# Performance work log

Measured on AMD Instinct MI355X. Metric: run time of the kernel, lower is better.

The kernel has to match this reference:

```python
import jax, jax.numpy as jnp
import numpy as np

B, C, N, IC = 4, 64, 4096, 32  # batch, in_channels(=g_channels), nodes, inter_channels


def setup_inputs() -> dict:
    key = jax.random.key(0)
    ks = jax.random.split(key, 8)
    s_c = (2.0 / C) ** 0.5   # kaiming-ish scales
    s_i = (2.0 / C) ** 0.5
    x = jax.random.normal(ks[0], (B, C, N), dtype=jnp.float32)
    g_w = jax.random.normal(ks[1], (C, C), dtype=jnp.float32) * s_c      # g: 1x1 conv (out=C, in=C)
    g_b = jnp.zeros((C,), dtype=jnp.float32)
    theta_w = jax.random.normal(ks[2], (IC, C), dtype=jnp.float32) * s_i  # theta: (out=IC, in=C)
    theta_b = jnp.zeros((IC,), dtype=jnp.float32)
    phi_w = jax.random.normal(ks[3], (IC, C), dtype=jnp.float32) * s_i
    phi_b = jnp.zeros((IC,), dtype=jnp.float32)
    cp_w = jax.random.normal(ks[4], (2 * IC,), dtype=jnp.float32) * (2.0 / (2 * IC)) ** 0.5  # concat_project 1x1 conv, no bias
    C_k = jnp.zeros((N, N), dtype=jnp.float32)  # learned adjacency bias, init zeros
    return {"x": x, "g_w": g_w, "g_b": g_b, "theta_w": theta_w, "theta_b": theta_b,
            "phi_w": phi_w, "phi_b": phi_b, "cp_w": cp_w, "C_k": C_k}


def reference(x, g_w, g_b, theta_w, theta_b, phi_w, phi_b, cp_w, C_k):
    # 1x1 convs are plain GEMMs over the node dim
    g_x = jnp.einsum('oc,bcn->bno', g_w, x) + g_b            # (B, N, C)
    th = jnp.einsum('oc,bcn->bon', theta_w, x) + theta_b[:, None]  # (B, IC, N)
    ph = jnp.einsum('oc,bcn->bon', phi_w, x) + phi_b[:, None]      # (B, IC, N)
    # concat_project on [theta_i ; phi_j] with a 1x1 conv is algebraically an outer sum:
    # f[b,i,j] = w_th . theta[b,:,i] + w_ph . phi[b,:,j]
    a = jnp.einsum('c,bcn->bn', cp_w[:IC], th)  # (B, N)
    p = jnp.einsum('c,bcn->bn', cp_w[IC:], ph)  # (B, N)
    f = a[:, :, None] + p[:, None, :]           # (B, N, N)
    attention = jax.nn.softmax(jax.nn.leaky_relu(f, negative_slope=0.2), axis=-1) + C_k
    y = jnp.einsum('bij,bjo->boi', attention, g_x)  # (B, C, N)
    return y
```

## Files before the change

kernel.cpp:

```cpp
#include <hip/hip_runtime.h>


#define B  4
#define C  64
#define N  4096
#define IC 32
#define NS 4104
#define MAGIC 0x13572468

#define OFF_FLAG   248
#define OFF_A      256
#define OFF_P      (OFF_A + B*N)
#define OFF_Q      (OFF_P + B*N)
#define OFF_PERM   (OFF_Q + B*N)
#define OFF_PRES   (OFF_PERM + B*N)
#define OFF_SUFS   (OFF_PRES + B*NS)
#define OFF_S1     (OFF_SUFS + B*NS)
#define OFF_S2     (OFF_S1 + B*64*64)
#define OFF_GX     (OFF_S2 + B*64*64)
#define OFF_GS1    (OFF_GX + B*N*64)
#define OFF_GS2    (OFF_GS1 + B*N*64)

__global__ __launch_bounds__(256) void k1_gx(
    const float* __restrict__ x, const float* __restrict__ g_w,
    const float* __restrict__ g_b, const float* __restrict__ theta_w,
    const float* __restrict__ theta_b, const float* __restrict__ phi_w,
    const float* __restrict__ phi_b, const float* __restrict__ cp_w,
    const float* __restrict__ Ck, float* __restrict__ ws) {
  __shared__ float gwT[C * C];
  __shared__ float xl[C * 16];
  __shared__ float lu[C], lv[C], cst[2];
  const int tid = threadIdx.x;
  const int b = blockIdx.x >> 8;
  const int n0 = (blockIdx.x & 255) << 4;
  for (int idx = tid; idx < C * C; idx += 256) {
    int o = idx >> 6, cc = idx & 63;
    gwT[cc * C + o] = g_w[idx];
  }
  for (int idx = tid; idx < C * 16; idx += 256) {
    int cc = idx >> 4, nn = idx & 15;
    xl[idx] = x[(size_t)((b << 6) + cc) * N + n0 + nn];
  }
  if (tid < 64) {
    float u = 0.f;
    for (int k = 0; k < IC; ++k) u += cp_w[k] * theta_w[k * C + tid];
    lu[tid] = u;
  } else if (tid < 128) {
    int c = tid - 64;
    float v = 0.f;
    for (int k = 0; k < IC; ++k) v += cp_w[IC + k] * phi_w[k * C + c];
    lv[c] = v;
  } else if (tid == 128) {
    float ca = 0.f, cp2 = 0.f;
    for (int k = 0; k < IC; ++k) { ca += cp_w[k] * theta_b[k]; cp2 += cp_w[IC + k] * phi_b[k]; }
    cst[0] = ca; cst[1] = cp2;
  }
  __syncthreads();
  if (tid < 16) {
    float au = cst[0], pu = cst[1];
    for (int cc = 0; cc < C; ++cc) {
      float xv = xl[cc * 16 + tid];
      au += lu[cc] * xv;
      pu += lv[cc] * xv;
    }
    ws[OFF_A + (b << 12) + n0 + tid] = au;
    ws[OFF_P + (b << 12) + n0 + tid] = pu;
  }
  const int o = tid & 63, g4 = tid >> 6;
  float bb = g_b[o];
  float acc0 = bb, acc1 = bb, acc2 = bb, acc3 = bb;
  for (int cc = 0; cc < C; ++cc) {
    float gv = gwT[cc * C + o];
    const float* xr = &xl[cc * 16 + (g4 << 2)];
    acc0 += gv * xr[0]; acc1 += gv * xr[1]; acc2 += gv * xr[2]; acc3 += gv * xr[3];
  }
  float* gx = ws + OFF_GX + (size_t)((b << 12) + n0 + (g4 << 2)) * C + o;
  gx[0] = acc0; gx[64] = acc1; gx[128] = acc2; gx[192] = acc3;
  const float4* c4 = (const float4*)Ck;
  bool nz = false;
  int idx = (blockIdx.x << 8) + tid;
  for (int t = 0; t < 16; ++t) {
    float4 v = c4[idx];
    nz |= (v.x != 0.f) | (v.y != 0.f) | (v.z != 0.f) | (v.w != 0.f);
    idx += 262144;
  }
  if (__any(nz) && (tid & 63) == 0)
    atomicExch((int*)ws + OFF_FLAG, MAGIC);
}

__global__ __launch_bounds__(1024) void k2_rank(float* __restrict__ ws) {
  __shared__ float lp[N];
  __shared__ int partials[32][33];
  const int tid = threadIdx.x;
  const int b = blockIdx.x >> 7;
  const int rg = blockIdx.x & 127;
  const float* p = ws + OFF_P + b * N;
  ((float4*)lp)[tid] = ((const float4*)p)[tid];
  const int row = tid & 31, chunk = tid >> 5;
  const int i = (rg << 5) + row;
  __syncthreads();
  const float my = lp[i];
  const int c0 = chunk << 7;
  const float4* lp4 = (const float4*)(lp + c0);
  int r0 = 0, r1 = 0, r2 = 0, r3 = 0;
  for (int j = 0; j < 32; ++j) {
    float4 v = lp4[j];
    int k = c0 + (j << 2);
    r0 += (v.x < my) || (v.x == my && (k + 0) < i);
    r1 += (v.y < my) || (v.y == my && (k + 1) < i);
    r2 += (v.z < my) || (v.z == my && (k + 2) < i);
    r3 += (v.w < my) || (v.w == my && (k + 3) < i);
  }
  partials[row][chunk] = (r0 + r1) + (r2 + r3);
  __syncthreads();
  if (tid < 32) {
    int rank = 0;
#pragma unroll
    for (int c = 0; c < 32; ++c) rank += partials[tid][c];
    const int ii = (rg << 5) + tid;
    ws[OFF_Q + (b << 12) + rank] = lp[ii];
    ((int*)ws)[OFF_PERM + (b << 12) + rank] = ii;
  }
}

__global__ __launch_bounds__(1024) void k3_sums(float* __restrict__ ws) {
  __shared__ float sA[1024], sB[1024];
  const int tid = threadIdx.x;
  const int bid = blockIdx.x;
  if (bid < B * 64) {
    const int b = bid >> 6, c = bid & 63;
    const int o = tid & 63, kk = tid >> 6;
    const float* q = ws + OFF_Q + b * N;
    const int* perm = (const int*)ws + OFF_PERM + b * N;
    const float* gx = ws + OFF_GX + ((size_t)b << 18);
    float* gs1 = ws + OFF_GS1 + ((size_t)b << 18);
    float* gs2 = ws + OFF_GS2 + ((size_t)b << 18);
    float p1 = 0.f, p2 = 0.f;
    const int k0 = (c << 6) + (kk << 2);
    for (int r = 0; r < 4; ++r) {
      int k = k0 + r;
      float qv = q[k];
      float e1v = expf(qv), e2v = expf(0.2f * qv);
      float g = gx[((size_t)perm[k] << 6) + o];
      float w1 = e1v * g, w2 = e2v * g;
      gs1[((size_t)k << 6) + o] = w1;
      gs2[((size_t)k << 6) + o] = w2;
      p1 += w1; p2 += w2;
    }
    sA[(kk << 6) + o] = p2;
    sB[(kk << 6) + o] = p1;
    __syncthreads();
    if (tid < 64) {
      float t2 = 0.f, t1 = 0.f;
#pragma unroll
      for (int g2 = 0; g2 < 16; ++g2) { t2 += sA[(g2 << 6) + o]; t1 += sB[(g2 << 6) + o]; }
      ws[OFF_S2 + (size_t)(((b << 6) + c) << 6) + o] = t2;
      ws[OFF_S1 + (size_t)(((b << 6) + c) << 6) + o] = t1;
    }
  } else {
    const int b = bid - B * 64;
    float* wt2 = sA;
    float* wt1 = sA + 16;
    float* wo2 = sA + 32;
    float* wo1 = sA + 49;
    const float* q = ws + OFF_Q + b * N;
    const float4 qv4 = ((const float4*)q)[tid];
    float e1r[4], e2r[4];
    e2r[0] = expf(0.2f * qv4.x); e1r[0] = expf(qv4.x);
    e2r[1] = expf(0.2f * qv4.y); e1r[1] = expf(qv4.y);
    e2r[2] = expf(0.2f * qv4.z); e1r[2] = expf(qv4.z);
    e2r[3] = expf(0.2f * qv4.w); e1r[3] = expf(qv4.w);
    float s2 = e2r[0] + e2r[1] + e2r[2] + e2r[3];
    float s1 = e1r[0] + e1r[1] + e1r[2] + e1r[3];
    const int lane = tid & 63, wave = tid >> 6;
    float x2 = s2, x1 = s1;
    for (int off = 1; off < 64; off <<= 1) {
      float t2 = __shfl_up(x2, off, 64);
      float t1 = __shfl_up(x1, off, 64);
      if (lane >= off) { x2 += t2; x1 += t1; }
    }
    if (lane == 63) { wt2[wave] = x2; wt1[wave] = x1; }
    __syncthreads();
    if (wave == 0 && lane < 17) {
      float a2 = 0.f, a1 = 0.f;
      for (int w = 0; w < 16; ++w) {
        if (w < lane) { a2 += wt2[w]; a1 += wt1[w]; }
      }
      wo2[lane] = a2; wo1[lane] = a1;
    }
    __syncthreads();
    const float excl2 = wo2[wave] + (x2 - s2);
    const float incl1 = wo1[wave] + x1;
    const float tot1 = wo1[16];
    float* PreS = ws + OFF_PRES + b * NS;
    float* SufS = ws + OFF_SUFS + b * NS;
    const int base = tid << 2;
    float run = excl2;
#pragma unroll
    for (int j = 0; j < 4; ++j) { PreS[base + j] = run; run += e2r[j]; }
    if (tid == 1023) PreS[N] = run;
    run = tot1 - incl1;
#pragma unroll
    for (int j = 3; j >= 0; --j) { run += e1r[j]; SufS[base + j] = run; }
    if (tid == 1023) SufS[N] = 0.f;
  }
}

__global__ __launch_bounds__(1024) void k4_out(const float* __restrict__ Ck,
                                               float* __restrict__ ws,
                                               float* __restrict__ y) {
  __shared__ float lqy[4224];
  __shared__ float offP[4096];
  __shared__ float offS[4096];
  const int tid = threadIdx.x;
  const int b = blockIdx.x >> 6, rg = blockIdx.x & 63;
  float* lq = lqy;
  ((float4*)lq)[tid] = ((const float4*)(ws + OFF_Q + b * N))[tid];
  if (tid < 64) {
    const float* S2g = ws + OFF_S2 + ((size_t)b << 12);
    float run = 0.f;
    for (int c2 = 0; c2 < 64; ++c2) { offP[(c2 << 6) + tid] = run; run += S2g[(c2 << 6) + tid]; }
  } else if (tid < 128) {
    const int o = tid - 64;
    const float* S1g = ws + OFF_S1 + ((size_t)b << 12);
    float run = 0.f;
    for (int c2 = 63; c2 >= 0; --c2) { offS[(c2 << 6) + o] = run; run += S1g[(c2 << 6) + o]; }
  }
  __syncthreads();
  const int wave = tid >> 6, lane = tid & 63;
  int r_k[4], r_ce[4];
  float r_e1[4], r_e2[4], r_inv[4];
#pragma unroll
  for (int rr = 0; rr < 4; ++rr) {
    const int row = (wave << 2) + rr;
    const int i = (rg << 6) + row;
    const float ai = ws[OFF_A + (b << 12) + i];
    const float thr = -ai;
    int lo = 0, hi = N;
    while (lo < hi) { int m = (lo + hi) >> 1; if (lq[m] <= thr) lo = m + 1; else hi = m; }
    r_k[rr] = lo;
    r_ce[rr] = min(lo >> 6, 63);
    r_e1[rr] = expf(ai);
    r_e2[rr] = expf(0.2f * ai);
    float den = r_e1[rr] * ws[OFF_SUFS + b * NS + lo] +
                r_e2[rr] * ws[OFF_PRES + b * NS + lo];
    r_inv[rr] = 1.0f / den;
  }
  __syncthreads();
  float* yblk = lqy;
  const float* gs1 = ws + OFF_GS1 + ((size_t)b << 18) + lane;
  const float* gs2 = ws + OFF_GS2 + ((size_t)b << 18) + lane;
#pragma unroll
  for (int rr = 0; rr < 4; ++rr) {
    const int row = (wave << 2) + rr;
    const int ce = r_ce[rr], j0 = ce << 6, m = r_k[rr] - j0;
    const float* g2p = gs2 + ((size_t)j0 << 6);
    const float* g1p = gs1 + ((size_t)j0 << 6);
    float a0 = 0.f, a1 = 0.f, a2 = 0.f, a3 = 0.f;
    float b0 = 0.f, b1 = 0.f, b2 = 0.f, b3 = 0.f;
    int j = 0;
    for (; j + 4 <= m; j += 4) {
      a0 += g2p[(size_t)(j + 0) << 6];
      a1 += g2p[(size_t)(j + 1) << 6];
      a2 += g2p[(size_t)(j + 2) << 6];
      a3 += g2p[(size_t)(j + 3) << 6];
    }
    for (; j < m; ++j) a0 += g2p[(size_t)j << 6];
    for (; j + 4 <= 64; j += 4) {
      b0 += g1p[(size_t)(j + 0) << 6];
      b1 += g1p[(size_t)(j + 1) << 6];
      b2 += g1p[(size_t)(j + 2) << 6];
      b3 += g1p[(size_t)(j + 3) << 6];
    }
    for (; j < 64; ++j) b0 += g1p[(size_t)j << 6];
    float accA = (a0 + a1) + (a2 + a3);
    float accB = (b0 + b1) + (b2 + b3);
    float num = r_e1[rr] * (offS[(ce << 6) + lane] + accB) +
                r_e2[rr] * (offP[(ce << 6) + lane] + accA);
    yblk[row * 65 + lane] = num * r_inv[rr];
  }
  __syncthreads();
  {
    const int i = lane, o0 = wave << 2;
#pragma unroll
    for (int rr = 0; rr < 4; ++rr) {
      int o = o0 + rr;
      y[((size_t)((b << 6) + o)) * N + (rg << 6) + i] = yblk[i * 65 + o];
    }
  }
  if (((const volatile int*)ws)[OFF_FLAG] == MAGIC) {
    __syncthreads();
    const int o = tid & 63, jj = tid >> 6;
    const float* gxb = ws + OFF_GX + ((size_t)b << 18);
    float (*red)[64] = (float(*)[64])lqy;
    for (int ii = 0; ii < 64; ++ii) {
      int irow = (rg << 6) + ii;
      float acc2 = 0.f;
      for (int j = jj; j < N; j += 16)
        acc2 += Ck[(size_t)irow * N + j] * gxb[((size_t)j << 6) + o];
      red[jj][o] = acc2;
      __syncthreads();
      if (jj == 0) {
        float s = 0.f;
#pragma unroll
        for (int g2 = 0; g2 < 16; ++g2) s += red[g2][o];
        y[((size_t)((b << 6) + o)) * N + irow] += s;
      }
      __syncthreads();
    }
  }
}

extern "C" void kernel_launch(void* const* d_in, const int* in_sizes, int n_in,
                              void* d_out, int out_size, void* d_ws, size_t ws_size,
                              hipStream_t stream) {
  (void)in_sizes; (void)n_in; (void)out_size; (void)ws_size;
  const float* x       = (const float*)d_in[0];
  const float* g_w     = (const float*)d_in[1];
  const float* g_b     = (const float*)d_in[2];
  const float* theta_w = (const float*)d_in[3];
  const float* theta_b = (const float*)d_in[4];
  const float* phi_w   = (const float*)d_in[5];
  const float* phi_b   = (const float*)d_in[6];
  const float* cp_w    = (const float*)d_in[7];
  const float* Ck      = (const float*)d_in[8];
  float* ws = (float*)d_ws;
  float* y  = (float*)d_out;

  hipLaunchKernelGGL(k1_gx, dim3(1024), dim3(256), 0, stream,
                     x, g_w, g_b, theta_w, theta_b, phi_w, phi_b, cp_w, Ck, ws);
  hipLaunchKernelGGL(k2_rank, dim3(512), dim3(1024), 0, stream, ws);
  hipLaunchKernelGGL(k3_sums, dim3(B * 64 + B), dim3(1024), 0, stream, ws);
  hipLaunchKernelGGL(k4_out, dim3(B * 64), dim3(1024), 0, stream, Ck, ws, y);
}
```

Baseline: 170.2 us.

## Fuse weighted-gx scatter and chunk sums into rank kernel, drop k3

```diff
diff --git a/kernel.cpp b/kernel.cpp
--- a/kernel.cpp
+++ b/kernel.cpp
@@ -5,17 +5,15 @@
 #define C  64
 #define N  4096
 #define IC 32
-#define NS 4104
 #define MAGIC 0x13572468
 
 #define OFF_FLAG   248
 #define OFF_A      256
 #define OFF_P      (OFF_A + B*N)
 #define OFF_Q      (OFF_P + B*N)
-#define OFF_PERM   (OFF_Q + B*N)
-#define OFF_PRES   (OFF_PERM + B*N)
-#define OFF_SUFS   (OFF_PRES + B*NS)
-#define OFF_S1     (OFF_SUFS + B*NS)
+#define OFF_ES1    (OFF_Q + B*N)
+#define OFF_ES2    (OFF_ES1 + B*N)
+#define OFF_S1     (OFF_ES2 + B*N)
 #define OFF_S2     (OFF_S1 + B*64*64)
 #define OFF_GX     (OFF_S2 + B*64*64)
 #define OFF_GS1    (OFF_GX + B*N*64)
@@ -33,6 +31,8 @@
   const int tid = threadIdx.x;
   const int b = blockIdx.x >> 8;
   const int n0 = (blockIdx.x & 255) << 4;
+  if (blockIdx.x < 128)
+    ws[OFF_S1 + (blockIdx.x << 8) + tid] = 0.f;
   for (int idx = tid; idx < C * C; idx += 256) {
     int o = idx >> 6, cc = idx & 63;
     gwT[cc * C + o] = g_w[idx];
@@ -91,6 +91,7 @@
 __global__ __launch_bounds__(1024) void k2_rank(float* __restrict__ ws) {
   __shared__ float lp[N];
   __shared__ int partials[32][33];
+  __shared__ int rankL[32];
   const int tid = threadIdx.x;
   const int b = blockIdx.x >> 7;
   const int rg = blockIdx.x & 127;
@@ -117,118 +118,83 @@
     int rank = 0;
 #pragma unroll
     for (int c = 0; c < 32; ++c) rank += partials[tid][c];
+    rankL[tid] = rank;
     const int ii = (rg << 5) + tid;
-    ws[OFF_Q + (b << 12) + rank] = lp[ii];
-    ((int*)ws)[OFF_PERM + (b << 12) + rank] = ii;
-  }
-}
-
-__global__ __launch_bounds__(1024) void k3_sums(float* __restrict__ ws) {
-  __shared__ float sA[1024], sB[1024];
-  const int tid = threadIdx.x;
-  const int bid = blockIdx.x;
-  if (bid < B * 64) {
-    const int b = bid >> 6, c = bid & 63;
-    const int o = tid & 63, kk = tid >> 6;
-    const float* q = ws + OFF_Q + b * N;
-    const int* perm = (const int*)ws + OFF_PERM + b * N;
-    const float* gx = ws + OFF_GX + ((size_t)b << 18);
-    float* gs1 = ws + OFF_GS1 + ((size_t)b << 18);
-    float* gs2 = ws + OFF_GS2 + ((size_t)b << 18);
-    float p1 = 0.f, p2 = 0.f;
-    const int k0 = (c << 6) + (kk << 2);
-    for (int r = 0; r < 4; ++r) {
-      int k = k0 + r;
-      float qv = q[k];
-      float e1v = expf(qv), e2v = expf(0.2f * qv);
-      float g = gx[((size_t)perm[k] << 6) + o];
-      float w1 = e1v * g, w2 = e2v * g;
-      gs1[((size_t)k << 6) + o] = w1;
-      gs2[((size_t)k << 6) + o] = w2;
-      p1 += w1; p2 += w2;
-    }
-    sA[(kk << 6) + o] = p2;
-    sB[(kk << 6) + o] = p1;
-    __syncthreads();
-    if (tid < 64) {
-      float t2 = 0.f, t1 = 0.f;
-#pragma unroll
-      for (int g2 = 0; g2 < 16; ++g2) { t2 += sA[(g2 << 6) + o]; t1 += sB[(g2 << 6) + o]; }
-      ws[OFF_S2 + (size_t)(((b << 6) + c) << 6) + o] = t2;
-      ws[OFF_S1 + (size_t)(((b << 6) + c) << 6) + o] = t1;
-    }
-  } else {
-    const int b = bid - B * 64;
-    float* wt2 = sA;
-    float* wt1 = sA + 16;
-    float* wo2 = sA + 32;
-    float* wo1 = sA + 49;
-    const float* q = ws + OFF_Q + b * N;
-    const float4 qv4 = ((const float4*)q)[tid];
-    float e1r[4], e2r[4];
-    e2r[0] = expf(0.2f * qv4.x); e1r[0] = expf(qv4.x);
-    e2r[1] = expf(0.2f * qv4.y); e1r[1] = expf(qv4.y);
-    e2r[2] = expf(0.2f * qv4.z); e1r[2] = expf(qv4.z);
-    e2r[3] = expf(0.2f * qv4.w); e1r[3] = expf(qv4.w);
-    float s2 = e2r[0] + e2r[1] + e2r[2] + e2r[3];
-    float s1 = e1r[0] + e1r[1] + e1r[2] + e1r[3];
-    const int lane = tid & 63, wave = tid >> 6;
-    float x2 = s2, x1 = s1;
-    for (int off = 1; off < 64; off <<= 1) {
-      float t2 = __shfl_up(x2, off, 64);
-      float t1 = __shfl_up(x1, off, 64);
-      if (lane >= off) { x2 += t2; x1 += t1; }
-    }
-    if (lane == 63) { wt2[wave] = x2; wt1[wave] = x1; }
-    __syncthreads();
-    if (wave == 0 && lane < 17) {
-      float a2 = 0.f, a1 = 0.f;
-      for (int w = 0; w < 16; ++w) {
-        if (w < lane) { a2 += wt2[w]; a1 += wt1[w]; }
-      }
-      wo2[lane] = a2; wo1[lane] = a1;
-    }
-    __syncthreads();
-    const float excl2 = wo2[wave] + (x2 - s2);
-    const float incl1 = wo1[wave] + x1;
-    const float tot1 = wo1[16];
-    float* PreS = ws + OFF_PRES + b * NS;
-    float* SufS = ws + OFF_SUFS + b * NS;
-    const int base = tid << 2;
-    float run = excl2;
-#pragma unroll
-    for (int j = 0; j < 4; ++j) { PreS[base + j] = run; run += e2r[j]; }
-    if (tid == 1023) PreS[N] = run;
-    run = tot1 - incl1;
-#pragma unroll
-    for (int j = 3; j >= 0; --j) { run += e1r[j]; SufS[base + j] = run; }
-    if (tid == 1023) SufS[N] = 0.f;
+    float pv = lp[ii];
+    ws[OFF_Q + (b << 12) + rank] = pv;
+    ws[OFF_ES1 + (b << 12) + rank] = expf(pv);
+    ws[OFF_ES2 + (b << 12) + rank] = expf(0.2f * pv);
+  }
+  __syncthreads();
+  const int lane = tid & 63, wave = tid >> 6;
+  const float* gx = ws + OFF_GX + ((size_t)b << 18);
+  float* gs1 = ws + OFF_GS1 + ((size_t)b << 18);
+  float* gs2 = ws + OFF_GS2 + ((size_t)b << 18);
+  float* S1g = ws + OFF_S1 + (b << 12);
+  float* S2g = ws + OFF_S2 + (b << 12);
+  for (int r = wave; r < 32; r += 16) {
+    const int ii = (rg << 5) + r;
+    float pv = lp[ii];
+    float e1v = expf(pv), e2v = expf(0.2f * pv);
+    float g = gx[((size_t)ii << 6) + lane];
+    const int rk = rankL[r];
+    float w1 = e1v * g, w2 = e2v * g;
+    gs1[((size_t)rk << 6) + lane] = w1;
+    gs2[((size_t)rk << 6) + lane] = w2;
+    atomicAdd(&S1g[((rk >> 6) << 6) + lane], w1);
+    atomicAdd(&S2g[((rk >> 6) << 6) + lane], w2);
   }
 }
 
 __global__ __launch_bounds__(1024) void k4_out(const float* __restrict__ Ck,
                                                float* __restrict__ ws,
                                                float* __restrict__ y) {
-  __shared__ float lqy[4224];
+  __shared__ float lqd[4224];
+  __shared__ float les1[4096], les2[4096];
   __shared__ float offP[4096];
   __shared__ float offS[4096];
+  __shared__ float csum1[64], csum2[64], offPS[64], offSS[64];
   const int tid = threadIdx.x;
   const int b = blockIdx.x >> 6, rg = blockIdx.x & 63;
-  float* lq = lqy;
-  ((float4*)lq)[tid] = ((const float4*)(ws + OFF_Q + b * N))[tid];
+  ((float4*)lqd)[tid]  = ((const float4*)(ws + OFF_Q  + (b << 12)))[tid];
+  ((float4*)les1)[tid] = ((const float4*)(ws + OFF_ES1 + (b << 12)))[tid];
+  ((float4*)les2)[tid] = ((const float4*)(ws + OFF_ES2 + (b << 12)))[tid];
+  ((float4*)offP)[tid] = ((const float4*)(ws + OFF_S2 + (b << 12)))[tid];
+  ((float4*)offS)[tid] = ((const float4*)(ws + OFF_S1 + (b << 12)))[tid];
+  __syncthreads();
   if (tid < 64) {
-    const float* S2g = ws + OFF_S2 + ((size_t)b << 12);
     float run = 0.f;
-    for (int c2 = 0; c2 < 64; ++c2) { offP[(c2 << 6) + tid] = run; run += S2g[(c2 << 6) + tid]; }
+    for (int c = 0; c < 64; ++c) {
+      float t = offP[(c << 6) + tid]; offP[(c << 6) + tid] = run; run += t;
+    }
   } else if (tid < 128) {
     const int o = tid - 64;
-    const float* S1g = ws + OFF_S1 + ((size_t)b << 12);
     float run = 0.f;
-    for (int c2 = 63; c2 >= 0; --c2) { offS[(c2 << 6) + o] = run; run += S1g[(c2 << 6) + o]; }
+    for (int c = 63; c >= 0; --c) {
+      float t = offS[(c << 6) + o]; offS[(c << 6) + o] = run; run += t;
+    }
+  } else if (tid < 192) {
+    const int c = tid - 128;
+    float s = 0.f;
+    for (int j = 0; j < 64; ++j) s += les1[(c << 6) + ((j + c) & 63)];
+    csum1[c] = s;
+  } else if (tid < 256) {
+    const int c = tid - 192;
+    float s = 0.f;
+    for (int j = 0; j < 64; ++j) s += les2[(c << 6) + ((j + c) & 63)];
+    csum2[c] = s;
+  }
+  __syncthreads();
+  if (tid == 0) {
+    float run = 0.f;
+    for (int c = 0; c < 64; ++c) { offPS[c] = run; run += csum2[c]; }
+  } else if (tid == 1) {
+    float run = 0.f;
+    for (int c = 63; c >= 0; --c) { offSS[c] = run; run += csum1[c]; }
   }
   __syncthreads();
   const int wave = tid >> 6, lane = tid & 63;
-  int r_k[4], r_ce[4];
+  int r_ce[4], r_m[4];
   float r_e1[4], r_e2[4], r_inv[4];
 #pragma unroll
   for (int rr = 0; rr < 4; ++rr) {
@@ -237,23 +203,24 @@
     const float ai = ws[OFF_A + (b << 12) + i];
     const float thr = -ai;
     int lo = 0, hi = N;
-    while (lo < hi) { int m = (lo + hi) >> 1; if (lq[m] <= thr) lo = m + 1; else hi = m; }
-    r_k[rr] = lo;
-    r_ce[rr] = min(lo >> 6, 63);
-    r_e1[rr] = expf(ai);
-    r_e2[rr] = expf(0.2f * ai);
-    float den = r_e1[rr] * ws[OFF_SUFS + b * NS + lo] +
-                r_e2[rr] * ws[OFF_PRES + b * NS + lo];
-    r_inv[rr] = 1.0f / den;
-  }
-  __syncthreads();
-  float* yblk = lqy;
+    while (lo < hi) { int m = (lo + hi) >> 1; if (lqd[m] <= thr) lo = m + 1; else hi = m; }
+    const int ce = min(lo >> 6, 63);
+    const int j0 = ce << 6, m = lo - j0;
+    const float e1 = expf(ai), e2 = expf(0.2f * ai);
+    float d2 = 0.f, d1 = 0.f;
+    for (int j = 0; j < m; ++j) d2 += les2[j0 + j];
+    for (int j = m; j < 64; ++j) d1 += les1[j0 + j];
+    r_ce[rr] = ce; r_m[rr] = m; r_e1[rr] = e1; r_e2[rr] = e2;
+    r_inv[rr] = 1.0f / (e1 * (offSS[ce] + d1) + e2 * (offPS[ce] + d2));
+  }
+  __syncthreads();
+  float* yblk = lqd;
   const float* gs1 = ws + OFF_GS1 + ((size_t)b << 18) + lane;
   const float* gs2 = ws + OFF_GS2 + ((size_t)b << 18) + lane;
 #pragma unroll
   for (int rr = 0; rr < 4; ++rr) {
     const int row = (wave << 2) + rr;
-    const int ce = r_ce[rr], j0 = ce << 6, m = r_k[rr] - j0;
+    const int ce = r_ce[rr], j0 = ce << 6, m = r_m[rr];
     const float* g2p = gs2 + ((size_t)j0 << 6);
     const float* g1p = gs1 + ((size_t)j0 << 6);
     float a0 = 0.f, a1 = 0.f, a2 = 0.f, a3 = 0.f;
@@ -292,7 +259,7 @@
     __syncthreads();
     const int o = tid & 63, jj = tid >> 6;
     const float* gxb = ws + OFF_GX + ((size_t)b << 18);
-    float (*red)[64] = (float(*)[64])lqy;
+    float (*red)[64] = (float(*)[64])lqd;
     for (int ii = 0; ii < 64; ++ii) {
       int irow = (rg << 6) + ii;
       float acc2 = 0.f;
@@ -330,6 +297,5 @@
   hipLaunchKernelGGL(k1_gx, dim3(1024), dim3(256), 0, stream,
                      x, g_w, g_b, theta_w, theta_b, phi_w, phi_b, cp_w, Ck, ws);
   hipLaunchKernelGGL(k2_rank, dim3(512), dim3(1024), 0, stream, ws);
-  hipLaunchKernelGGL(k3_sums, dim3(B * 64 + B), dim3(1024), 0, stream, ws);
   hipLaunchKernelGGL(k4_out, dim3(B * 64), dim3(1024), 0, stream, Ck, ws, y);
 }
```

Result: slower. 178.3 us (+4.7%).
